# Performance work log

Measured on AMD Instinct MI355X. Metric: run time of the kernel, lower is better.

## Reference

```python
import jax, jax.numpy as jnp
import numpy as np
from functools import partial

DN = jax.lax.conv_dimension_numbers((1, 1, 3, 3), (1, 1, 3, 3), ('NCHW', 'OIHW', 'NCHW'))


def setup_inputs() -> dict:
    key = jax.random.key(0)
    ks = jax.random.split(key, 5)
    x = jax.random.normal(ks[0], (16, 1, 512, 512), dtype=jnp.float32)
    k = jax.random.normal(ks[1], (1, 1, 3, 3), dtype=jnp.float32)
    w1 = jax.random.normal(ks[2], (10, 1), dtype=jnp.float32) * 0.5
    b1 = jax.random.normal(ks[3], (10,), dtype=jnp.float32) * 0.1
    w2 = jax.random.normal(ks[4], (1, 10), dtype=jnp.float32) * 0.5
    return {"x": x, "k": k, "w1": w1, "b1": b1, "w2": w2, "steps": 16}


def _step(x, k, w1, b1, w2):
    # 3x3 stencil, 1 channel, SAME padding, no bias
    out = jax.lax.conv_general_dilated(x, k, (1, 1), 'SAME', dimension_numbers=DN)
    # gaussian activation
    out = jnp.exp(-(out - 1.0) ** 2)
    # pointwise MLP: 1 -> 10 (ReLU) -> 1 (Sigmoid)
    h = jax.nn.relu(jnp.einsum('bchw,oc->bohw', out, w1) + b1[None, :, None, None])
    out = jax.nn.sigmoid(jnp.einsum('bchw,oc->bohw', h, w2))
    # residual update
    return x + (out - 0.5)


def reference(x, k, w1, b1, w2, steps):
    def body(x, _):
        x_new = _step(x, k, w1, b1, w2)
        return x_new, x_new

    _, seq = jax.lax.scan(body, x, None, length=steps)
    # prepend initial state: [steps+1, B, 1, H, W]
    return jnp.concatenate([x[None], seq], axis=0)
```

## Files before the change

kernel.cpp:

```cpp
#include <hip/hip_runtime.h>


#define NCA_H 512
#define NCA_W 512
#define NCA_HW (NCA_H * NCA_W)
#define TX 80
#define HALO 8
#define NG 20

#define LOADR(W, rrow) do {                                                  \
    const float4 q_ = *(const float4*)(cb + (rrow) * TX + w0);               \
    W[1] = q_.x; W[2] = q_.y; W[3] = q_.z; W[4] = q_.w;                      \
    W[0] = __shfl_up(q_.w, 1);                                               \
    W[5] = __shfl_down(q_.x, 1);                                             \
} while (0)

#define COMPR(Wm, Wc, Wp, rrow) do {                                         \
    const int rr_ = (rrow);                                                  \
    const bool ok_ = colIn && ((unsigned)(gh0 + rr_) < NCA_H);               \
    float4 res_; float* rp_ = (float*)&res_;                                 \
    _Pragma("unroll")                                                        \
    for (int j = 0; j < 4; ++j) {                                            \
        float s_ = 0.f;                                                      \
        s_ = fmaf(kk[0], Wm[j],     s_);                                     \
        s_ = fmaf(kk[1], Wm[j + 1], s_);                                     \
        s_ = fmaf(kk[2], Wm[j + 2], s_);                                     \
        s_ = fmaf(kk[3], Wc[j],     s_);                                     \
        s_ = fmaf(kk[4], Wc[j + 1], s_);                                     \
        s_ = fmaf(kk[5], Wc[j + 2], s_);                                     \
        s_ = fmaf(kk[6], Wp[j],     s_);                                     \
        s_ = fmaf(kk[7], Wp[j + 1], s_);                                     \
        s_ = fmaf(kk[8], Wp[j + 2], s_);                                     \
        float d_ = s_ - 1.0f;                                                \
        float g_ = __expf(-d_ * d_);                                         \
        float a_ = 0.f;                                                      \
        _Pragma("unroll")                                                    \
        for (int o = 0; o < 10; ++o) {                                       \
            float h_ = fmaxf(fmaf(rw1[o], g_, rb1[o]), 0.f);                 \
            a_ = fmaf(rw2[o], h_, a_);                                       \
        }                                                                    \
        float sg_ = __fdividef(1.0f, 1.0f + __expf(-a_));                    \
        float v_ = Wc[j + 1] + (sg_ - 0.5f);                                 \
        rp_[j] = ok_ ? v_ : 0.f;                                             \
    }                                                                        \
    *(float4*)&nb[rr_ * TX + w0] = res_;                                     \
    if (colStore && rr_ >= HALO && rr_ < TX - HALO)                          \
        *(float4*)(gout + (size_t)(gh0 + rr_) * NCA_W + (gw0 + w0)) = res_;  \
} while (0)

__global__ __launch_bounds__(256, 3) void nca_fused(
        const float* __restrict__ src,
        float* __restrict__ traj,
        size_t slice, int nsteps, int writeInit,
        const float* __restrict__ kc, const float* __restrict__ w1v,
        const float* __restrict__ b1v, const float* __restrict__ w2v) {
    __shared__ float buf[2][TX * TX];

    float kk[9];
#pragma unroll
    for (int i = 0; i < 9; ++i) kk[i] = kc[i];
    float rw1[10], rb1[10], rw2[10];
#pragma unroll
    for (int o = 0; o < 10; ++o) { rw1[o] = w1v[o]; rb1[o] = b1v[o]; rw2[o] = w2v[o]; }

    const int bi = blockIdx.x;
    const int b  = bi >> 6;
    const int ty = (bi >> 3) & 7;
    const int tx = bi & 7;
    const int gh0 = ty * 64 - HALO;
    const int gw0 = tx * 64 - HALO;

    const float* sp = src + (size_t)b * NCA_HW;
    float* ip = traj + (size_t)b * NCA_HW;
    for (int i = threadIdx.x; i < (TX * TX / 4); i += 256) {
        int row = i / NG;
        int c4  = i - row * NG;
        int gh  = gh0 + row;
        int gw  = gw0 + 4 * c4;
        float4 v = make_float4(0.f, 0.f, 0.f, 0.f);
        if (((unsigned)gh < NCA_H) && ((unsigned)gw < NCA_W))
            v = *(const float4*)(sp + (size_t)gh * NCA_W + gw);
        *(float4*)&buf[0][4 * i] = v;
        if (writeInit && row >= HALO && row < TX - HALO &&
            c4 >= (HALO / 4) && c4 < (TX - HALO) / 4)
            *(float4*)(ip + (size_t)gh * NCA_W + gw) = v;
    }
    if (threadIdx.x < 2 * NG) {
        int row = (threadIdx.x < NG) ? 0 : (TX - 1);
        int c4  = threadIdx.x % NG;
        *(float4*)&buf[1][row * TX + 4 * c4] = make_float4(0.f, 0.f, 0.f, 0.f);
    }
    __syncthreads();

    const int tid  = threadIdx.x;
    const int lane = tid & 63;
    const int wid  = tid >> 6;
    const bool active = lane < 60;
    const int g    = lane % 20;
    const int sidx = wid * 3 + lane / 20;
    const int w0   = g * 4;
    const int r0   = (sidx < 6) ? (1 + 7 * sidx) : (43 + 6 * (sidx - 6));
    const bool n7  = (sidx < 6);
    const bool colStore = active && (w0 >= HALO) && (w0 < TX - HALO);
    const bool colIn = ((unsigned)(gw0 + w0) < NCA_W);

    int cur = 0;
    for (int s = 1; s <= nsteps; ++s) {
        const float* cb = buf[cur];
        float* nb = buf[cur ^ 1];
        float* gout = traj + (size_t)s * slice + (size_t)b * NCA_HW;
        if (active) {
            float A[6], B[6], C[6], D[6];
            LOADR(A, r0 - 1); LOADR(B, r0);
            LOADR(C, r0 + 1); LOADR(D, r0 + 2);
            COMPR(A, B, C, r0);       LOADR(A, r0 + 3);
            COMPR(B, C, D, r0 + 1);   LOADR(B, r0 + 4);
            COMPR(C, D, A, r0 + 2);   LOADR(C, r0 + 5);
            COMPR(D, A, B, r0 + 3);   LOADR(D, r0 + 6);
            COMPR(A, B, C, r0 + 4);
            COMPR(B, C, D, r0 + 5);
            if (n7) { LOADR(A, r0 + 7); COMPR(C, D, A, r0 + 6); }
        }
        __syncthreads();
        cur ^= 1;
    }
}

extern "C" void kernel_launch(void* const* d_in, const int* in_sizes, int n_in,
                              void* d_out, int out_size, void* d_ws, size_t ws_size,
                              hipStream_t stream) {
    const float* x  = (const float*)d_in[0];
    const float* k  = (const float*)d_in[1];
    const float* w1 = (const float*)d_in[2];
    const float* b1 = (const float*)d_in[3];
    const float* w2 = (const float*)d_in[4];
    float* out = (float*)d_out;

    const size_t slice = (size_t)in_sizes[0];
    const int steps = out_size / (int)slice - 1;
    const int B = (int)(slice / NCA_HW);

    const int blocks = B * 64;
    for (int base = 0; base < steps; base += HALO) {
        int ns = steps - base;
        if (ns > HALO) ns = HALO;
        const float* s0 = (base == 0) ? x : (out + (size_t)base * slice);
        nca_fused<<<blocks, 256, 0, stream>>>(s0, out + (size_t)base * slice,
                                              slice, ns, (base == 0) ? 1 : 0,
                                              k, w1, b1, w2);
    }
}
```

Baseline: 453.6 us.

## Use single LDS buffer with register-held results and split barriers

Replaces the double-buffered shared tile with one buffer. Each thread keeps its computed rows in registers, waits at a barrier, then writes them back to LDS and global memory before a second barrier. This halves LDS use so launch bounds can allow 4 blocks per CU instead of 3, and the __syncthreads calls become raw s_barrier calls preceded by an lgkmcnt wait. The cost is a second barrier per step, higher register pressure from holding 7 float4 results, and global stores that are grouped after compute rather than interleaved with it.

```diff
diff --git a/kernel.cpp b/kernel.cpp
--- a/kernel.cpp
+++ b/kernel.cpp
@@ -8,17 +8,23 @@
 #define HALO 8
 #define NG 20
 
+#define BAR() do {                                             \
+    asm volatile("s_waitcnt lgkmcnt(0)" ::: "memory");         \
+    __builtin_amdgcn_s_barrier();                              \
+    asm volatile("" ::: "memory");                             \
+} while (0)
+
 #define LOADR(W, rrow) do {                                                  \
-    const float4 q_ = *(const float4*)(cb + (rrow) * TX + w0);               \
+    const float4 q_ = *(const float4*)(buf + (rrow) * TX + w0);              \
     W[1] = q_.x; W[2] = q_.y; W[3] = q_.z; W[4] = q_.w;                      \
     W[0] = __shfl_up(q_.w, 1);                                               \
     W[5] = __shfl_down(q_.x, 1);                                             \
 } while (0)
 
-#define COMPR(Wm, Wc, Wp, rrow) do {                                         \
+#define COMPR(Wm, Wc, Wp, rrow, Rd) do {                                     \
     const int rr_ = (rrow);                                                  \
     const bool ok_ = colIn && ((unsigned)(gh0 + rr_) < NCA_H);               \
-    float4 res_; float* rp_ = (float*)&res_;                                 \
+    float* rp_ = (float*)&(Rd);                                              \
     _Pragma("unroll")                                                        \
     for (int j = 0; j < 4; ++j) {                                            \
         float s_ = 0.f;                                                      \
@@ -43,18 +49,22 @@
         float v_ = Wc[j + 1] + (sg_ - 0.5f);                                 \
         rp_[j] = ok_ ? v_ : 0.f;                                             \
     }                                                                        \
-    *(float4*)&nb[rr_ * TX + w0] = res_;                                     \
-    if (colStore && rr_ >= HALO && rr_ < TX - HALO)                          \
-        *(float4*)(gout + (size_t)(gh0 + rr_) * NCA_W + (gw0 + w0)) = res_;  \
 } while (0)
 
-__global__ __launch_bounds__(256, 3) void nca_fused(
+#define SROW(Rv, rrow) do {                                                  \
+    const int rr_ = (rrow);                                                  \
+    *(float4*)&buf[rr_ * TX + w0] = (Rv);                                    \
+    if (colStore && rr_ >= HALO && rr_ < TX - HALO)                          \
+        *(float4*)(gout + (size_t)(gh0 + rr_) * NCA_W + (gw0 + w0)) = (Rv);  \
+} while (0)
+
+__global__ __launch_bounds__(256, 4) void nca_fused(
         const float* __restrict__ src,
         float* __restrict__ traj,
         size_t slice, int nsteps, int writeInit,
         const float* __restrict__ kc, const float* __restrict__ w1v,
         const float* __restrict__ b1v, const float* __restrict__ w2v) {
-    __shared__ float buf[2][TX * TX];
+    __shared__ float buf[TX * TX];
 
     float kk[9];
 #pragma unroll
@@ -80,17 +90,12 @@
         float4 v = make_float4(0.f, 0.f, 0.f, 0.f);
         if (((unsigned)gh < NCA_H) && ((unsigned)gw < NCA_W))
             v = *(const float4*)(sp + (size_t)gh * NCA_W + gw);
-        *(float4*)&buf[0][4 * i] = v;
+        *(float4*)&buf[4 * i] = v;
         if (writeInit && row >= HALO && row < TX - HALO &&
             c4 >= (HALO / 4) && c4 < (TX - HALO) / 4)
             *(float4*)(ip + (size_t)gh * NCA_W + gw) = v;
     }
-    if (threadIdx.x < 2 * NG) {
-        int row = (threadIdx.x < NG) ? 0 : (TX - 1);
-        int c4  = threadIdx.x % NG;
-        *(float4*)&buf[1][row * TX + 4 * c4] = make_float4(0.f, 0.f, 0.f, 0.f);
-    }
-    __syncthreads();
+    BAR();
 
     const int tid  = threadIdx.x;
     const int lane = tid & 63;
@@ -104,25 +109,29 @@
     const bool colStore = active && (w0 >= HALO) && (w0 < TX - HALO);
     const bool colIn = ((unsigned)(gw0 + w0) < NCA_W);
 
-    int cur = 0;
     for (int s = 1; s <= nsteps; ++s) {
-        const float* cb = buf[cur];
-        float* nb = buf[cur ^ 1];
         float* gout = traj + (size_t)s * slice + (size_t)b * NCA_HW;
+        float4 R0, R1, R2, R3, R4, R5, R6;
         if (active) {
             float A[6], B[6], C[6], D[6];
             LOADR(A, r0 - 1); LOADR(B, r0);
             LOADR(C, r0 + 1); LOADR(D, r0 + 2);
-            COMPR(A, B, C, r0);       LOADR(A, r0 + 3);
-            COMPR(B, C, D, r0 + 1);   LOADR(B, r0 + 4);
-            COMPR(C, D, A, r0 + 2);   LOADR(C, r0 + 5);
-            COMPR(D, A, B, r0 + 3);   LOADR(D, r0 + 6);
-            COMPR(A, B, C, r0 + 4);
-            COMPR(B, C, D, r0 + 5);
-            if (n7) { LOADR(A, r0 + 7); COMPR(C, D, A, r0 + 6); }
+            COMPR(A, B, C, r0,     R0);  LOADR(A, r0 + 3);
+            COMPR(B, C, D, r0 + 1, R1);  LOADR(B, r0 + 4);
+            COMPR(C, D, A, r0 + 2, R2);  LOADR(C, r0 + 5);
+            COMPR(D, A, B, r0 + 3, R3);  LOADR(D, r0 + 6);
+            COMPR(A, B, C, r0 + 4, R4);
+            COMPR(B, C, D, r0 + 5, R5);
+            if (n7) { LOADR(A, r0 + 7); COMPR(C, D, A, r0 + 6, R6); }
         }
-        __syncthreads();
-        cur ^= 1;
+        BAR();
+        if (active) {
+            SROW(R0, r0);     SROW(R1, r0 + 1);
+            SROW(R2, r0 + 2); SROW(R3, r0 + 3);
+            SROW(R4, r0 + 4); SROW(R5, r0 + 5);
+            if (n7) SROW(R6, r0 + 6);
+        }
+        BAR();
     }
 }
 
```

New measurement: 448.6 us. Within noise of the previous version (-1.1%).
